# Optimization experiments

Hardware: AMD Instinct MI355X
Metric: run time of the kernel (lower is better)

The kernel has to match this reference:

```python
import jax, jax.numpy as jnp
import numpy as np

B, S, D, E, H = 4, 4096, 1024, 8, 128  # batch, seq, d_model, experts, expert hidden (hardcoded 128)


def setup_inputs() -> dict:
    key = jax.random.key(0)
    ks = jax.random.split(key, 7)
    s_in = 1.0 / np.sqrt(D)
    s_h = 1.0 / np.sqrt(H)
    return {
        "x": jax.random.normal(ks[0], (B, S, D), dtype=jnp.float32),
        "W1": jax.random.normal(ks[1], (E, D, H), dtype=jnp.float32) * s_in,
        "b1": jax.random.normal(ks[2], (E, H), dtype=jnp.float32) * s_in,
        "W2": jax.random.normal(ks[3], (E, H, D), dtype=jnp.float32) * s_h,
        "b2": jax.random.normal(ks[4], (E, D), dtype=jnp.float32) * s_h,
        "Wg": jax.random.normal(ks[5], (D, E), dtype=jnp.float32) * s_in,
        "bg": jax.random.normal(ks[6], (E,), dtype=jnp.float32) * s_in,
    }


def reference(x, W1, b1, W2, b2, Wg, bg):
    # Gate: softmax over experts. [B,S,E]
    gate = jax.nn.softmax(jnp.einsum("bsd,de->bse", x, Wg) + bg, axis=-1)
    # Dense per-expert MLP applied to every token.
    h = jax.nn.relu(jnp.einsum("bsd,edh->bseh", x, W1) + b1)          # [B,S,E,H]
    y = jnp.einsum("bseh,eho->bseo", h, W2) + b2                       # [B,S,E,D]
    # Fused weighted sum over the expert axis (replaces the python double loop).
    out = jnp.einsum("bse,bseo->bso", gate, y)                         # [B,S,D]
    return out
```

## Files before the change

kernel.cpp:

```cpp
#include <hip/hip_runtime.h>
#include <hip/hip_bf16.h>

#define B_ 4
#define S_ 4096
#define D_ 1024
#define E_ 8
#define H_ 128
#define M_ (B_*S_)
#define K_ 1024
#define N_ 1024
#define NT_ (K_/64)
#define NIT_ (NT_/2)

typedef short bf16x8 __attribute__((ext_vector_type(8)));
typedef float f32x4 __attribute__((ext_vector_type(4)));

__device__ __forceinline__ unsigned short f2bf(float f){
  union { float f; unsigned int u; } v; v.f = f;
  unsigned int u = v.u;
  unsigned int r = (u + 0x7fffu + ((u >> 16) & 1u)) >> 16;
  return (unsigned short)r;
}

__device__ __forceinline__ void gload16(const void* g, void* l){
  __builtin_amdgcn_global_load_lds((const __attribute__((address_space(1))) void*)g,
                                   (__attribute__((address_space(3))) void*)l, 16, 0, 0);
}

__global__ __launch_bounds__(256)
void prep_x_gate(const float* __restrict__ x, const float* __restrict__ Wg,
                 const float* __restrict__ bg, unsigned short* __restrict__ xb,
                 float* __restrict__ gate){
  int tid = threadIdx.x;
  int lane = tid & 63;
  int m = blockIdx.x * 4 + (tid >> 6);
  const float* xr = x + (size_t)m * D_;
  unsigned short* xbr = xb + (size_t)m * D_;
  float acc[E_];
  #pragma unroll
  for (int e = 0; e < E_; ++e) acc[e] = 0.f;
  #pragma unroll
  for (int c = 0; c < D_/64; ++c){
    int d = c*64 + lane;
    float xs = xr[d];
    xbr[d] = f2bf(xs);
    const float4 w0 = *(const float4*)(Wg + (size_t)d * E_);
    const float4 w1 = *(const float4*)(Wg + (size_t)d * E_ + 4);
    acc[0] = fmaf(xs, w0.x, acc[0]); acc[1] = fmaf(xs, w0.y, acc[1]);
    acc[2] = fmaf(xs, w0.z, acc[2]); acc[3] = fmaf(xs, w0.w, acc[3]);
    acc[4] = fmaf(xs, w1.x, acc[4]); acc[5] = fmaf(xs, w1.y, acc[5]);
    acc[6] = fmaf(xs, w1.z, acc[6]); acc[7] = fmaf(xs, w1.w, acc[7]);
  }
  #pragma unroll
  for (int off = 32; off > 0; off >>= 1){
    #pragma unroll
    for (int e = 0; e < E_; ++e) acc[e] += __shfl_xor(acc[e], off, 64);
  }
  float lg[E_]; float mx = -1e30f;
  #pragma unroll
  for (int e = 0; e < E_; ++e){ lg[e] = acc[e] + bg[e]; mx = fmaxf(mx, lg[e]); }
  float s = 0.f;
  #pragma unroll
  for (int e = 0; e < E_; ++e){ lg[e] = expf(lg[e] - mx); s += lg[e]; }
  float inv = 1.f / s;
  if (lane < E_) gate[(size_t)m * E_ + lane] = lg[lane] * inv;
}

__global__ __launch_bounds__(256)
void transpose_pack(const float* __restrict__ in, unsigned short* __restrict__ out,
                    int C, int ostride, int in_estride, int out_ebase){
  __shared__ float t[32][33];
  int e = blockIdx.z;
  const float* ip = in + (size_t)e * in_estride;
  unsigned short* op = out + (size_t)e * out_ebase;
  int tx = threadIdx.x, ty = threadIdx.y;
  int c0 = blockIdx.x * 32, r0 = blockIdx.y * 32;
  #pragma unroll
  for (int yy = 0; yy < 32; yy += 8)
    t[ty + yy][tx] = ip[(size_t)(r0 + ty + yy) * C + (c0 + tx)];
  __syncthreads();
  #pragma unroll
  for (int yy = 0; yy < 32; yy += 8)
    op[(size_t)(c0 + ty + yy) * ostride + (r0 + tx)] = f2bf(t[tx][ty + yy]);
}

template<int PASS>
__global__ __launch_bounds__(512, 2)
void gemm_moe8(const unsigned short* __restrict__ A,
               const unsigned short* __restrict__ Bt,
               const float* __restrict__ gate,
               const float* __restrict__ bias,
               void* __restrict__ outp)
{
  __shared__ unsigned short lds[65536];

  int bid = blockIdx.x;
  int xcd = bid & 7, pos = bid >> 3;
  int mb = xcd * 8 + (pos >> 2);
  int nb = pos & 3;
  int m0 = mb * 256, n0 = nb * 256;

  int tid = threadIdx.x;
  int lane = tid & 63;
  int w = tid >> 6;
  int wm = w & 1, wn = w >> 1;
  int rowi = lane & 15, s4 = lane >> 4;

  int sg = (tid & 7) ^ ((tid >> 3) & 7);
  const unsigned short* gA = A  + (size_t)(m0 + (tid >> 3)) * K_ + sg * 8;
  const unsigned short* gB = Bt + (size_t)(n0 + (tid >> 3)) * K_ + sg * 8;
  int t8 = tid * 8;

#define STAGE_A(b,h,kt) do{ const unsigned short* g_ = gA + (size_t)((h)*128)*K_ + (kt)*64; \
  gload16(g_,                 &lds[(b)*16384 + (h)*8192 + t8]); \
  gload16(g_ + (size_t)64*K_, &lds[(b)*16384 + (h)*8192 + t8 + 4096]); }while(0)
#define STAGE_B(b,h,kt) do{ const unsigned short* g_ = gB + (size_t)((h)*128)*K_ + (kt)*64; \
  gload16(g_,                 &lds[32768 + (b)*16384 + (h)*8192 + t8]); \
  gload16(g_ + (size_t)64*K_, &lds[32768 + (b)*16384 + (h)*8192 + t8 + 4096]); }while(0)

  int bk0 = rowi*64 + (( s4     ) ^ (rowi & 7)) * 8;
  int bk1 = rowi*64 + ((4 + s4  ) ^ (rowi & 7)) * 8;
  int abase0 = wm * 8192;
  int bbase0 = 32768 + (wn >> 1) * 8192 + (wn & 1) * 4096;

  f32x4 acc[8][4];
  #pragma unroll
  for (int i = 0; i < 8; ++i){
    #pragma unroll
    for (int j = 0; j < 4; ++j){ f32x4 z = {0.f,0.f,0.f,0.f}; acc[i][j] = z; }
  }
  bf16x8 af[4][2], bfr[4][2];

#define READ_A(b,r) do{ int ab_ = (b)*16384 + abase0; \
  _Pragma("unroll") for (int f2 = 0; f2 < 4; ++f2){ \
    af[f2][0] = *(const bf16x8*)&lds[ab_ + ((r)*4+f2)*1024 + bk0]; \
    af[f2][1] = *(const bf16x8*)&lds[ab_ + ((r)*4+f2)*1024 + bk1]; } }while(0)
#define READ_B(b,c) do{ int bb_ = (b)*16384 + bbase0; \
  _Pragma("unroll") for (int j2 = 0; j2 < 2; ++j2){ \
    bfr[(c)*2+j2][0] = *(const bf16x8*)&lds[bb_ + ((c)*2+j2)*1024 + bk0]; \
    bfr[(c)*2+j2][1] = *(const bf16x8*)&lds[bb_ + ((c)*2+j2)*1024 + bk1]; } }while(0)
#define MFMA16(r,c) do{ \
  _Pragma("unroll") for (int f2 = 0; f2 < 4; ++f2) \
  _Pragma("unroll") for (int j2 = 0; j2 < 2; ++j2){ \
    acc[(r)*4+f2][(c)*2+j2] = __builtin_amdgcn_mfma_f32_16x16x32_bf16(af[f2][0], bfr[(c)*2+j2][0], acc[(r)*4+f2][(c)*2+j2], 0,0,0); \
    acc[(r)*4+f2][(c)*2+j2] = __builtin_amdgcn_mfma_f32_16x16x32_bf16(af[f2][1], bfr[(c)*2+j2][1], acc[(r)*4+f2][(c)*2+j2], 0,0,0); \
  } }while(0)

#define PH_MID  __builtin_amdgcn_s_barrier(); \
                asm volatile("s_waitcnt lgkmcnt(0)" ::: "memory"); \
                __builtin_amdgcn_s_setprio(1)
#define PH_END  __builtin_amdgcn_s_setprio(0); __builtin_amdgcn_s_barrier()
#define PH_END_VM(N) __builtin_amdgcn_s_setprio(0); \
                asm volatile("s_waitcnt vmcnt(" #N ")" ::: "memory"); \
                __builtin_amdgcn_s_barrier()

  STAGE_B(0,0,0); STAGE_B(0,1,0);
  STAGE_A(0,0,0); STAGE_A(0,1,0);
  STAGE_B(1,0,1); STAGE_B(1,1,1);
  STAGE_A(1,0,1);
  asm volatile("s_waitcnt vmcnt(6)" ::: "memory");
  __builtin_amdgcn_s_barrier();

  #pragma unroll 1
  for (int it = 0; it < NIT_; ++it){
    int kt1  = 2*it + 1;
    int ktn0 = 2*it + 2, ktn1 = 2*it + 3;
    bool more = (it < NIT_ - 1);
    READ_A(0,0); READ_B(0,0);
    STAGE_A(1,1,kt1);
    PH_MID; MFMA16(0,0); PH_END;
    READ_B(0,1);
    PH_MID; MFMA16(0,1); PH_END;
    READ_A(0,1);
    if (more) STAGE_B(0,0,ktn0);
    PH_MID; MFMA16(1,1); PH_END;
    if (more) STAGE_B(0,1,ktn0);
    PH_MID; MFMA16(1,0);
    __builtin_amdgcn_s_setprio(0);
    if (more) { asm volatile("s_waitcnt vmcnt(4)" ::: "memory"); }
    else      { asm volatile("s_waitcnt vmcnt(0)" ::: "memory"); }
    __builtin_amdgcn_s_barrier();
    READ_A(1,0); READ_B(1,0);
    if (more) STAGE_A(0,0,ktn0);
    PH_MID; MFMA16(0,0); PH_END;
    READ_B(1,1);
    if (more) STAGE_A(0,1,ktn0);
    PH_MID; MFMA16(0,1); PH_END;
    READ_A(1,1);
    if (more) STAGE_B(1,0,ktn1);
    PH_MID; MFMA16(1,1); PH_END;
    if (more){ STAGE_B(1,1,ktn1); STAGE_A(1,0,ktn1); }
    PH_MID; MFMA16(1,0); PH_END_VM(6);
  }

  float* lws = (float*)lds + w * 4096;
  int ncol0 = n0 + wn*64;

  if (PASS == 1){
    unsigned short* Hp = (unsigned short*)outp;
    int e = nb*2 + (wn >> 1);
    float b1v[4];
    #pragma unroll
    for (int j = 0; j < 4; ++j) b1v[j] = bias[e*H_ + (wn&1)*64 + j*16 + rowi];
    #pragma unroll
    for (int ci = 0; ci < 2; ++ci){
      #pragma unroll
      for (int f2 = 0; f2 < 4; ++f2){
        int fi = ci*4 + f2;
        #pragma unroll
        for (int jj = 0; jj < 4; ++jj){
          int m = m0 + wm*128 + fi*16 + s4*4 + jj;
          float g = gate[(size_t)m*E_ + e];
          int r_l = f2*16 + s4*4 + jj;
          #pragma unroll
          for (int j = 0; j < 4; ++j){
            float v = fmaxf(acc[fi][j][jj] + b1v[j], 0.f) * g;
            lws[r_l*64 + ((j*16 + rowi) ^ (s4 << 4))] = v;
          }
        }
      }
      asm volatile("s_waitcnt lgkmcnt(0)" ::: "memory");
      #pragma unroll
      for (int it2 = 0; it2 < 16; ++it2){
        int r_l = it2*4 + (lane >> 4);
        int c4  = lane & 15;
        int X   = it2 & 3;
        f32x4 v = *(const f32x4*)&lws[r_l*64 + ((c4*4) ^ (X << 4))];
        union { unsigned short us[4]; uint2 u2; } pk;
        #pragma unroll
        for (int q = 0; q < 4; ++q) pk.us[q] = f2bf(v[q]);
        int m = m0 + wm*128 + ci*64 + r_l;
        *(uint2*)&Hp[(size_t)m*N_ + ncol0 + c4*4] = pk.u2;
      }
      if (ci == 0) asm volatile("s_waitcnt lgkmcnt(0)" ::: "memory");
    }
  } else {
    float* Out = (float*)outp;
    float b2v[8][4];
    #pragma unroll
    for (int j = 0; j < 4; ++j){
      int n = ncol0 + j*16 + rowi;
      #pragma unroll
      for (int e = 0; e < 8; ++e) b2v[e][j] = bias[(size_t)e*N_ + n];
    }
    #pragma unroll
    for (int ci = 0; ci < 2; ++ci){
      #pragma unroll
      for (int f2 = 0; f2 < 4; ++f2){
        int fi = ci*4 + f2;
        #pragma unroll
        for (int jj = 0; jj < 4; ++jj){
          int m = m0 + wm*128 + fi*16 + s4*4 + jj;
          const float4 g0 = *(const float4*)(gate + (size_t)m*E_);
          const float4 g1 = *(const float4*)(gate + (size_t)m*E_ + 4);
          int r_l = f2*16 + s4*4 + jj;
          #pragma unroll
          for (int j = 0; j < 4; ++j){
            float bv = g0.x*b2v[0][j] + g0.y*b2v[1][j] + g0.z*b2v[2][j] + g0.w*b2v[3][j]
                     + g1.x*b2v[4][j] + g1.y*b2v[5][j] + g1.z*b2v[6][j] + g1.w*b2v[7][j];
            lws[r_l*64 + ((j*16 + rowi) ^ (s4 << 4))] = acc[fi][j][jj] + bv;
          }
        }
      }
      asm volatile("s_waitcnt lgkmcnt(0)" ::: "memory");
      #pragma unroll
      for (int it2 = 0; it2 < 16; ++it2){
        int r_l = it2*4 + (lane >> 4);
        int c4  = lane & 15;
        int X   = it2 & 3;
        f32x4 v = *(const f32x4*)&lws[r_l*64 + ((c4*4) ^ (X << 4))];
        int m = m0 + wm*128 + ci*64 + r_l;
        *(f32x4*)&Out[(size_t)m*N_ + ncol0 + c4*4] = v;
      }
      if (ci == 0) asm volatile("s_waitcnt lgkmcnt(0)" ::: "memory");
    }
  }
#undef STAGE_A
#undef STAGE_B
#undef READ_A
#undef READ_B
#undef MFMA16
#undef PH_MID
#undef PH_END
#undef PH_END_VM
}

extern "C" void kernel_launch(void* const* d_in, const int* in_sizes, int n_in,
                              void* d_out, int out_size, void* d_ws, size_t ws_size,
                              hipStream_t stream){
  const float* x  = (const float*)d_in[0];
  const float* W1 = (const float*)d_in[1];
  const float* b1 = (const float*)d_in[2];
  const float* W2 = (const float*)d_in[3];
  const float* b2 = (const float*)d_in[4];
  const float* Wg = (const float*)d_in[5];
  const float* bg = (const float*)d_in[6];
  float* out = (float*)d_out;

  char* ws = (char*)d_ws;
  unsigned short* xb  = (unsigned short*)(ws);
  unsigned short* Hp  = (unsigned short*)(ws + ((size_t)32<<20));
  unsigned short* B1T = (unsigned short*)(ws + ((size_t)64<<20));
  unsigned short* B2T = (unsigned short*)(ws + ((size_t)66<<20));
  float*          gate= (float*)(ws + ((size_t)68<<20));

  hipLaunchKernelGGL(prep_x_gate, dim3(M_/4), dim3(256), 0, stream, x, Wg, bg, xb, gate);
  hipLaunchKernelGGL(transpose_pack, dim3(128/32, 1024/32, 8), dim3(32,8), 0, stream,
                     W1, B1T, 128, 1024, 1024*128, 128*1024);
  hipLaunchKernelGGL(transpose_pack, dim3(1024/32, 128/32, 8), dim3(32,8), 0, stream,
                     W2, B2T, 1024, 1024, 128*1024, 128);
  hipLaunchKernelGGL((gemm_moe8<1>), dim3(256), dim3(512), 0, stream,
                     xb, B1T, gate, b1, (void*)Hp);
  hipLaunchKernelGGL((gemm_moe8<2>), dim3(256), dim3(512), 0, stream,
                     Hp, B2T, gate, b2, (void*)out);
}
```

Baseline: 107.4 us.

## Drop per-phase trailing barriers in GEMM loop and store pass-2 output directly

Removes the second s_barrier after each MFMA phase in the double-buffered GEMM main loop, relying on the barrier at the start of the next phase plus vmcnt waits moved before it. For pass 2 it also removes the LDS round-trip in the epilogue and writes fp32 results straight from accumulators to global memory with per-lane strided stores. This halves the barrier count per k-step, but the pass-2 stores become less coalesced (16 consecutive floats per row segment instead of 16-byte vector stores). The reduced synchronisation may risk LDS races if the remaining barriers do not cover buffer reuse.

```diff
diff --git a/kernel.cpp b/kernel.cpp
--- a/kernel.cpp
+++ b/kernel.cpp
@@ -83,53 +83,6 @@
   for (int yy = 0; yy < 32; yy += 8)
     op[(size_t)(c0 + ty + yy) * ostride + (r0 + tx)] = f2bf(t[tx][ty + yy]);
 }
-
-template<int PASS>
-__global__ __launch_bounds__(512, 2)
-void gemm_moe8(const unsigned short* __restrict__ A,
-               const unsigned short* __restrict__ Bt,
-               const float* __restrict__ gate,
-               const float* __restrict__ bias,
-               void* __restrict__ outp)
-{
-  __shared__ unsigned short lds[65536];
-
-  int bid = blockIdx.x;
-  int xcd = bid & 7, pos = bid >> 3;
-  int mb = xcd * 8 + (pos >> 2);
-  int nb = pos & 3;
-  int m0 = mb * 256, n0 = nb * 256;
-
-  int tid = threadIdx.x;
-  int lane = tid & 63;
-  int w = tid >> 6;
-  int wm = w & 1, wn = w >> 1;
-  int rowi = lane & 15, s4 = lane >> 4;
-
-  int sg = (tid & 7) ^ ((tid >> 3) & 7);
-  const unsigned short* gA = A  + (size_t)(m0 + (tid >> 3)) * K_ + sg * 8;
-  const unsigned short* gB = Bt + (size_t)(n0 + (tid >> 3)) * K_ + sg * 8;
-  int t8 = tid * 8;
-
-#define STAGE_A(b,h,kt) do{ const unsigned short* g_ = gA + (size_t)((h)*128)*K_ + (kt)*64; \
-  gload16(g_,                 &lds[(b)*16384 + (h)*8192 + t8]); \
-  gload16(g_ + (size_t)64*K_, &lds[(b)*16384 + (h)*8192 + t8 + 4096]); }while(0)
-#define STAGE_B(b,h,kt) do{ const unsigned short* g_ = gB + (size_t)((h)*128)*K_ + (kt)*64; \
-  gload16(g_,                 &lds[32768 + (b)*16384 + (h)*8192 + t8]); \
-  gload16(g_ + (size_t)64*K_, &lds[32768 + (b)*16384 + (h)*8192 + t8 + 4096]); }while(0)
-
-  int bk0 = rowi*64 + (( s4     ) ^ (rowi & 7)) * 8;
-  int bk1 = rowi*64 + ((4 + s4  ) ^ (rowi & 7)) * 8;
-  int abase0 = wm * 8192;
-  int bbase0 = 32768 + (wn >> 1) * 8192 + (wn & 1) * 4096;
-
-  f32x4 acc[8][4];
-  #pragma unroll
-  for (int i = 0; i < 8; ++i){
-    #pragma unroll
-    for (int j = 0; j < 4; ++j){ f32x4 z = {0.f,0.f,0.f,0.f}; acc[i][j] = z; }
-  }
-  bf16x8 af[4][2], bfr[4][2];
 
 #define READ_A(b,r) do{ int ab_ = (b)*16384 + abase0; \
   _Pragma("unroll") for (int f2 = 0; f2 < 4; ++f2){ \
@@ -145,20 +98,64 @@
     acc[(r)*4+f2][(c)*2+j2] = __builtin_amdgcn_mfma_f32_16x16x32_bf16(af[f2][0], bfr[(c)*2+j2][0], acc[(r)*4+f2][(c)*2+j2], 0,0,0); \
     acc[(r)*4+f2][(c)*2+j2] = __builtin_amdgcn_mfma_f32_16x16x32_bf16(af[f2][1], bfr[(c)*2+j2][1], acc[(r)*4+f2][(c)*2+j2], 0,0,0); \
   } }while(0)
-
 #define PH_MID  __builtin_amdgcn_s_barrier(); \
                 asm volatile("s_waitcnt lgkmcnt(0)" ::: "memory"); \
                 __builtin_amdgcn_s_setprio(1)
-#define PH_END  __builtin_amdgcn_s_setprio(0); __builtin_amdgcn_s_barrier()
-#define PH_END_VM(N) __builtin_amdgcn_s_setprio(0); \
-                asm volatile("s_waitcnt vmcnt(" #N ")" ::: "memory"); \
-                __builtin_amdgcn_s_barrier()
+#define PH_END  __builtin_amdgcn_s_setprio(0)
+#define VMW(N)  asm volatile("s_waitcnt vmcnt(" #N ")" ::: "memory")
+
+template<int PASS>
+__global__ __launch_bounds__(512, 2)
+void gemm_moe8(const unsigned short* __restrict__ A,
+               const unsigned short* __restrict__ Bt,
+               const float* __restrict__ gate,
+               const float* __restrict__ bias,
+               void* __restrict__ outp)
+{
+  __shared__ unsigned short lds[65536];
+
+  int bid = blockIdx.x;
+  int xcd = bid & 7, pos = bid >> 3;
+  int mb = xcd * 8 + (pos >> 2);
+  int nb = pos & 3;
+  int m0 = mb * 256, n0 = nb * 256;
+
+  int tid = threadIdx.x;
+  int lane = tid & 63;
+  int w = tid >> 6;
+  int wm = w & 1, wn = w >> 1;
+  int rowi = lane & 15, s4 = lane >> 4;
+
+  int sg = (tid & 7) ^ ((tid >> 3) & 7);
+  const unsigned short* gA = A  + (size_t)(m0 + (tid >> 3)) * K_ + sg * 8;
+  const unsigned short* gB = Bt + (size_t)(n0 + (tid >> 3)) * K_ + sg * 8;
+  int t8 = tid * 8;
+
+#define STAGE_A(b,h,kt) do{ const unsigned short* g_ = gA + (size_t)((h)*128)*K_ + (kt)*64; \
+  gload16(g_,                 &lds[(b)*16384 + (h)*8192 + t8]); \
+  gload16(g_ + (size_t)64*K_, &lds[(b)*16384 + (h)*8192 + t8 + 4096]); }while(0)
+#define STAGE_B(b,h,kt) do{ const unsigned short* g_ = gB + (size_t)((h)*128)*K_ + (kt)*64; \
+  gload16(g_,                 &lds[32768 + (b)*16384 + (h)*8192 + t8]); \
+  gload16(g_ + (size_t)64*K_, &lds[32768 + (b)*16384 + (h)*8192 + t8 + 4096]); }while(0)
+
+  int bk0 = rowi*64 + (( s4     ) ^ (rowi & 7)) * 8;
+  int bk1 = rowi*64 + ((4 + s4  ) ^ (rowi & 7)) * 8;
+  int abase0 = wm * 8192;
+  int bbase0 = 32768 + (wn >> 1) * 8192 + (wn & 1) * 4096;
+
+  f32x4 acc[8][4];
+  #pragma unroll
+  for (int i = 0; i < 8; ++i){
+    #pragma unroll
+    for (int j = 0; j < 4; ++j){ f32x4 z = {0.f,0.f,0.f,0.f}; acc[i][j] = z; }
+  }
+  bf16x8 af[4][2], bfr[4][2];
 
   STAGE_B(0,0,0); STAGE_B(0,1,0);
   STAGE_A(0,0,0); STAGE_A(0,1,0);
   STAGE_B(1,0,1); STAGE_B(1,1,1);
   STAGE_A(1,0,1);
-  asm volatile("s_waitcnt vmcnt(6)" ::: "memory");
+  VMW(6);
   __builtin_amdgcn_s_barrier();
 
   #pragma unroll 1
@@ -174,12 +171,9 @@
     READ_A(0,1);
     if (more) STAGE_B(0,0,ktn0);
     PH_MID; MFMA16(1,1); PH_END;
-    if (more) STAGE_B(0,1,ktn0);
-    PH_MID; MFMA16(1,0);
-    __builtin_amdgcn_s_setprio(0);
-    if (more) { asm volatile("s_waitcnt vmcnt(4)" ::: "memory"); }
-    else      { asm volatile("s_waitcnt vmcnt(0)" ::: "memory"); }
-    __builtin_amdgcn_s_barrier();
+    if (more){ STAGE_B(0,1,ktn0); VMW(4); }
+    else     { VMW(0); }
+    PH_MID; MFMA16(1,0); PH_END;
     READ_A(1,0); READ_B(1,0);
     if (more) STAGE_A(0,0,ktn0);
     PH_MID; MFMA16(0,0); PH_END;
@@ -190,14 +184,15 @@
     if (more) STAGE_B(1,0,ktn1);
     PH_MID; MFMA16(1,1); PH_END;
     if (more){ STAGE_B(1,1,ktn1); STAGE_A(1,0,ktn1); }
-    PH_MID; MFMA16(1,0); PH_END_VM(6);
-  }
-
-  float* lws = (float*)lds + w * 4096;
+    VMW(6);
+    PH_MID; MFMA16(1,0); PH_END;
+  }
+
   int ncol0 = n0 + wn*64;
-
   if (PASS == 1){
+    __builtin_amdgcn_s_barrier();
     unsigned short* Hp = (unsigned short*)outp;
+    float* lws = (float*)lds + w * 4096;
     int e = nb*2 + (wn >> 1);
     float b1v[4];
     #pragma unroll
@@ -224,8 +219,8 @@
       for (int it2 = 0; it2 < 16; ++it2){
         int r_l = it2*4 + (lane >> 4);
         int c4  = lane & 15;
-        int X   = it2 & 3;
-        f32x4 v = *(const f32x4*)&lws[r_l*64 + ((c4*4) ^ (X << 4))];
+        int X2  = it2 & 3;
+        f32x4 v = *(const f32x4*)&lws[r_l*64 + ((c4*4) ^ (X2 << 4))];
         union { unsigned short us[4]; uint2 u2; } pk;
         #pragma unroll
         for (int q = 0; q < 4; ++q) pk.us[q] = f2bf(v[q]);
@@ -244,45 +239,25 @@
       for (int e = 0; e < 8; ++e) b2v[e][j] = bias[(size_t)e*N_ + n];
     }
     #pragma unroll
-    for (int ci = 0; ci < 2; ++ci){
-      #pragma unroll
-      for (int f2 = 0; f2 < 4; ++f2){
-        int fi = ci*4 + f2;
-        #pragma unroll
-        for (int jj = 0; jj < 4; ++jj){
-          int m = m0 + wm*128 + fi*16 + s4*4 + jj;
-          const float4 g0 = *(const float4*)(gate + (size_t)m*E_);
-          const float4 g1 = *(const float4*)(gate + (size_t)m*E_ + 4);
-          int r_l = f2*16 + s4*4 + jj;
-          #pragma unroll
-          for (int j = 0; j < 4; ++j){
-            float bv = g0.x*b2v[0][j] + g0.y*b2v[1][j] + g0.z*b2v[2][j] + g0.w*b2v[3][j]
-                     + g1.x*b2v[4][j] + g1.y*b2v[5][j] + g1.z*b2v[6][j] + g1.w*b2v[7][j];
-            lws[r_l*64 + ((j*16 + rowi) ^ (s4 << 4))] = acc[fi][j][jj] + bv;
-          }
-        }
+    for (int fi = 0; fi < 8; ++fi){
+      #pragma unroll
+      for (int jj = 0; jj < 4; ++jj){
+        int m = m0 + wm*128 + fi*16 + s4*4 + jj;
+        const float4 g0 = *(const float4*)(gate + (size_t)m*E_);
+        const float4 g1 = *(const float4*)(gate + (size_t)m*E_ + 4);
+        float bv[4];
+        #pragma unroll
+        for (int j = 0; j < 4; ++j)
+          bv[j] = g0.x*b2v[0][j] + g0.y*b2v[1][j] + g0.z*b2v[2][j] + g0.w*b2v[3][j]
+                + g1.x*b2v[4][j] + g1.y*b2v[5][j] + g1.z*b2v[6][j] + g1.w*b2v[7][j];
+        #pragma unroll
+        for (int j = 0; j < 4; ++j)
+          Out[(size_t)m*N_ + ncol0 + j*16 + rowi] = acc[fi][j][jj] + bv[j];
       }
-      asm volatile("s_waitcnt lgkmcnt(0)" ::: "memory");
-      #pragma unroll
-      for (int it2 = 0; it2 < 16; ++it2){
-        int r_l = it2*4 + (lane >> 4);
-        int c4  = lane & 15;
-        int X   = it2 & 3;
-        f32x4 v = *(const f32x4*)&lws[r_l*64 + ((c4*4) ^ (X << 4))];
-        int m = m0 + wm*128 + ci*64 + r_l;
-        *(f32x4*)&Out[(size_t)m*N_ + ncol0 + c4*4] = v;
-      }
-      if (ci == 0) asm volatile("s_waitcnt lgkmcnt(0)" ::: "memory");
     }
   }
 #undef STAGE_A
 #undef STAGE_B
-#undef READ_A
-#undef READ_B
-#undef MFMA16
-#undef PH_MID
-#undef PH_END
-#undef PH_END_VM
 }
 
 extern "C" void kernel_launch(void* const* d_in, const int* in_sizes, int n_in,
```

New measurement: 101.7 us. 1.06x faster.
